# Optimization experiments

Measured on AMD Instinct MI355X. Metric: run time of the kernel, lower is better.

The kernel has to match this reference:

```python
import jax, jax.numpy as jnp
import numpy as np

N, IN, OUT, RANK = 8192, 4096, 4096, 16
SCALING = 2.0

def setup_inputs() -> dict:
    key = jax.random.key(0)
    k1, k2, k3, k4 = jax.random.split(key, 4)
    x = jax.random.normal(k1, (N, IN), dtype=jnp.float32)
    weight = jax.random.normal(k2, (OUT, IN), dtype=jnp.float32) * (1.0 / np.sqrt(IN))
    lora_A = jax.random.normal(k3, (RANK, IN), dtype=jnp.float32) * (1.0 / np.sqrt(IN))
    lora_B = jax.random.normal(k4, (OUT, RANK), dtype=jnp.float32) * 0.01
    return {"x": x, "weight": weight, "lora_A": lora_A, "lora_B": lora_B}

def reference(x, weight, lora_A, lora_B):
    # frozen base linear: F.linear(x, weight) == x @ weight.T  -> [N, OUT]
    base = jnp.einsum('ni,oi->no', x, weight)
    # LoRA branch: dropout(x) (p=0 => identity) @ A.T @ B.T, scaled
    lora = jnp.einsum('ni,ri->nr', x, lora_A)      # [N, RANK]
    lora = jnp.einsum('nr,or->no', lora, lora_B)   # [N, OUT]
    return base + lora * SCALING
```

## Files before the change

### kernel.cpp

```cpp
#include <hip/hip_runtime.h>


#define N_ROWS 8192
#define K_DIM  4096
#define N_COLS 4096
#define RANK   16
#define BK     64
#define NT     (K_DIM / BK)

typedef __bf16 bf16x8 __attribute__((ext_vector_type(8)));
typedef float  f32x4  __attribute__((ext_vector_type(4)));

__device__ __forceinline__ unsigned short f2bf(float f) {
  unsigned int u = __builtin_bit_cast(unsigned int, f);
  u += 0x7FFFu + ((u >> 16) & 1u);
  return (unsigned short)(u >> 16);
}


__global__ __launch_bounds__(256) void conv_x_kernel(const float* __restrict__ x,
                                                     unsigned short* __restrict__ xb) {
  size_t idx = (size_t)blockIdx.x * blockDim.x + threadIdx.x;
  const float4 v = *reinterpret_cast<const float4*>(x + idx * 4);
  ushort4 r;
  r.x = f2bf(v.x); r.y = f2bf(v.y); r.z = f2bf(v.z); r.w = f2bf(v.w);
  *reinterpret_cast<ushort4*>(xb + idx * 4) = r;
}

__global__ __launch_bounds__(256) void make_weff_kernel(const float* __restrict__ w,
                                                        const float* __restrict__ A,
                                                        const float* __restrict__ Bm,
                                                        unsigned short* __restrict__ wb) {
  size_t idx = (size_t)blockIdx.x * blockDim.x + threadIdx.x;
  int o  = (int)(idx >> 10);
  int ic = (int)(idx & 1023) << 2;
  const float4 wv = *reinterpret_cast<const float4*>(w + (size_t)o * K_DIM + ic);
  float a0 = wv.x, a1 = wv.y, a2 = wv.z, a3 = wv.w;
  float br[RANK];
#pragma unroll
  for (int r4 = 0; r4 < RANK / 4; ++r4) {
    const float4 bv = *reinterpret_cast<const float4*>(Bm + (size_t)o * RANK + r4 * 4);
    br[r4 * 4 + 0] = bv.x; br[r4 * 4 + 1] = bv.y;
    br[r4 * 4 + 2] = bv.z; br[r4 * 4 + 3] = bv.w;
  }
#pragma unroll
  for (int r = 0; r < RANK; ++r) {
    const float4 av = *reinterpret_cast<const float4*>(A + (size_t)r * K_DIM + ic);
    float b2 = br[r] * 2.0f;
    a0 += b2 * av.x; a1 += b2 * av.y; a2 += b2 * av.z; a3 += b2 * av.w;
  }
  ushort4 rr;
  rr.x = f2bf(a0); rr.y = f2bf(a1); rr.z = f2bf(a2); rr.w = f2bf(a3);
  *reinterpret_cast<ushort4*>(wb + (size_t)o * K_DIM + ic) = rr;
}


__device__ __forceinline__ void gload_lds16(const void* g, void* l) {
  __builtin_amdgcn_global_load_lds(
      (__attribute__((address_space(1))) void*)g,
      (__attribute__((address_space(3))) void*)l, 16, 0, 0);
}

__global__ __launch_bounds__(512, 1) void gemm_bf16_pipe(
    const unsigned short* __restrict__ xb, const unsigned short* __restrict__ wb,
    float* __restrict__ out) {
  __shared__ __align__(16) char smem[131072];

  const int t  = threadIdx.x;
  const int l  = t & 63;
  const int wv = t >> 6;
  const int lr = l & 15;
  const int lk = l >> 4;
  const int wr = wv >> 2;
  const int wc = wv & 3;

  const int bid  = blockIdx.x;
  const int sbid = (bid & 7) * 64 + (bid >> 3);
  const int bm   = sbid >> 4;
  const int bn   = sbid & 15;

  const int srow = t >> 3;
  const int scol = ((t & 7) ^ ((t >> 3) & 7)) << 3;
  const unsigned short* gA = xb + (size_t)(bm * 256 + srow) * K_DIM + scol;
  const unsigned short* gB = wb + (size_t)(bn * 256 + srow) * K_DIM + scol;
  char* ldsA = smem + t * 16;
  char* ldsB = smem + 65536 + t * 16;

#define STG_A(hh, SRC, NB) do {                                                 \
    const unsigned short* _g = (SRC) + (size_t)((hh) * 128) * K_DIM;            \
    char* _l = ldsA + (NB) + (hh) * 16384;                                      \
    gload_lds16(_g, _l);                                                        \
    gload_lds16(_g + (size_t)64 * K_DIM, _l + 8192);                            \
  } while (0)
#define STG_B(hh, SRC, NB) do {                                                 \
    const unsigned short* _g = (SRC) + (size_t)((hh) * 128) * K_DIM;            \
    char* _l = ldsB + (NB) + (hh) * 16384;                                      \
    gload_lds16(_g, _l);                                                        \
    gload_lds16(_g + (size_t)64 * K_DIM, _l + 8192);                            \
  } while (0)

  const int g0   = (lk ^ (lr & 7)) << 4;
  const int g1   = ((lk + 4) ^ (lr & 7)) << 4;
  const int aoff = (wr * 16 + lr) * 128;
  const int boff = (wc * 16 + lr) * 128;

  bf16x8 aE[8], aO[8], bO[4], bE[2][4];
  f32x4 acc[8][4];
#pragma unroll
  for (int m = 0; m < 8; ++m)
#pragma unroll
    for (int n = 0; n < 4; ++n)
      acc[m][n] = (f32x4){0.f, 0.f, 0.f, 0.f};

#define RD_A(DST, BASE) do {                                                    \
    _Pragma("unroll")                                                           \
    for (int m = 0; m < 4; ++m) {                                               \
      DST[2 * m + 0] = *(const bf16x8*)(smem + (BASE) + m * 4096 + aoff + g0);  \
      DST[2 * m + 1] = *(const bf16x8*)(smem + (BASE) + m * 4096 + aoff + g1);  \
    }                                                                           \
  } while (0)
#define RD_B(DST, BASE) do {                                                    \
    _Pragma("unroll")                                                           \
    for (int n = 0; n < 2; ++n) {                                               \
      DST[2 * n + 0] = *(const bf16x8*)(smem + 65536 + (BASE) + n * 8192 + boff + g0); \
      DST[2 * n + 1] = *(const bf16x8*)(smem + 65536 + (BASE) + n * 8192 + boff + g1); \
    }                                                                           \
  } while (0)

#define MFMA_Q(MB, AF, NB0, BF) do {                                            \
    _Pragma("unroll")                                                           \
    for (int mi = 0; mi < 4; ++mi)                                              \
      _Pragma("unroll")                                                         \
      for (int ni = 0; ni < 2; ++ni)                                            \
        _Pragma("unroll")                                                       \
        for (int kk = 0; kk < 2; ++kk)                                          \
          acc[(MB) + mi][(NB0) + ni] = __builtin_amdgcn_mfma_f32_16x16x32_bf16( \
              AF[mi * 2 + kk], BF[ni * 2 + kk], acc[(MB) + mi][(NB0) + ni], 0, 0, 0); \
  } while (0)

#define PH_BAR() do {                                                           \
    __builtin_amdgcn_sched_barrier(0);                                          \
    __builtin_amdgcn_s_barrier();                                               \
    __builtin_amdgcn_sched_barrier(0);                                          \
  } while (0)
#define PH_BAR_VM(VM) do {                                                      \
    __builtin_amdgcn_sched_barrier(0);                                          \
    asm volatile("s_waitcnt vmcnt(" #VM ")" ::: "memory");                      \
    __builtin_amdgcn_s_barrier();                                               \
    __builtin_amdgcn_sched_barrier(0);                                          \
  } while (0)

#define TILE(CB, NB, PC, PN, T) do {                                            \
    const int _tk = ((T) + 1 < NT) ? (T) + 1 : NT - 1;                          \
    const unsigned short* _sA = gA + (size_t)_tk * BK;                          \
    const unsigned short* _sB = gB + (size_t)_tk * BK;                          \
                                                                       \
    RD_B(bO, (CB) + 16384);                                                     \
    STG_A(0, _sA, NB); STG_A(1, _sA, NB);                                       \
    __builtin_amdgcn_s_setprio(1); MFMA_Q(0, aE, 0, bE[PC]);                    \
    __builtin_amdgcn_s_setprio(0);                                              \
    PH_BAR();                                                                   \
                                                                       \
    RD_A(aO, (CB) + 16384);                                                     \
    STG_B(0, _sB, NB); STG_B(1, _sB, NB);                                       \
    __builtin_amdgcn_s_setprio(1); MFMA_Q(0, aE, 2, bO);                        \
    __builtin_amdgcn_s_setprio(0);                                              \
    PH_BAR_VM(4);                                                               \
                                                                       \
    RD_A(aE, (NB));                                                             \
    __builtin_amdgcn_s_setprio(1); MFMA_Q(4, aO, 2, bO);                        \
    __builtin_amdgcn_s_setprio(0);                                              \
    PH_BAR_VM(2);                                                               \
                                                                       \
    RD_B(bE[PN], (NB));                                                         \
    __builtin_amdgcn_s_setprio(1); MFMA_Q(4, aO, 0, bE[PC]);                    \
    __builtin_amdgcn_s_setprio(0);                                              \
    PH_BAR_VM(0);                                                               \
  } while (0)

  STG_A(0, gA, 0); STG_A(1, gA, 0); STG_B(0, gB, 0); STG_B(1, gB, 0);
  __builtin_amdgcn_sched_barrier(0);
  asm volatile("s_waitcnt vmcnt(0)" ::: "memory");
  __builtin_amdgcn_s_barrier();
  __builtin_amdgcn_sched_barrier(0);
  RD_A(aE, 0);
  RD_B(bE[0], 0);

#pragma nounroll
  for (int u = 0; u < NT / 2; ++u) {
    TILE(0, 32768, 0, 1, 2 * u);
    TILE(32768, 0, 1, 0, 2 * u + 1);
  }

  const int orow = bm * 256 + wr * 16 + lk * 4;
  const int ocol = bn * 256 + wc * 16 + lr;
#pragma unroll
  for (int mf = 0; mf < 8; ++mf)
#pragma unroll
    for (int nf = 0; nf < 4; ++nf)
#pragma unroll
      for (int j = 0; j < 4; ++j)
        out[(size_t)(orow + mf * 32 + j) * N_COLS + (ocol + nf * 64)] = acc[mf][nf][j];

#undef STG_A
#undef STG_B
#undef RD_A
#undef RD_B
#undef MFMA_Q
#undef PH_BAR
#undef PH_BAR_VM
#undef TILE
}


__global__ __launch_bounds__(256) void fallback_kernel(const float* __restrict__ x,
                                                       const float* __restrict__ w,
                                                       const float* __restrict__ A,
                                                       const float* __restrict__ Bm,
                                                       float* __restrict__ out) {
  const int o    = blockIdx.x * 256 + threadIdx.x;
  const int nrow = blockIdx.y;
  float bro[RANK];
#pragma unroll
  for (int r = 0; r < RANK; ++r) bro[r] = Bm[(size_t)o * RANK + r] * 2.0f;
  float bacc = 0.f;
  float tacc[RANK];
#pragma unroll
  for (int r = 0; r < RANK; ++r) tacc[r] = 0.f;
  for (int k = 0; k < K_DIM; ++k) {
    float xv = x[(size_t)nrow * K_DIM + k];
    bacc += xv * w[(size_t)o * K_DIM + k];
#pragma unroll
    for (int r = 0; r < RANK; ++r) tacc[r] += xv * A[(size_t)r * K_DIM + k];
  }
  float res = bacc;
#pragma unroll
  for (int r = 0; r < RANK; ++r) res += bro[r] * tacc[r];
  out[(size_t)nrow * N_COLS + o] = res;
}


extern "C" void kernel_launch(void* const* d_in, const int* in_sizes, int n_in,
                              void* d_out, int out_size, void* d_ws, size_t ws_size,
                              hipStream_t stream) {
  const float* x  = (const float*)d_in[0];
  const float* w  = (const float*)d_in[1];
  const float* A  = (const float*)d_in[2];
  const float* Bm = (const float*)d_in[3];
  float* out = (float*)d_out;

  const size_t need = ((size_t)N_ROWS * K_DIM + (size_t)N_COLS * K_DIM) * sizeof(unsigned short);
  if (ws_size < need) {
    dim3 grid(N_COLS / 256, N_ROWS);
    fallback_kernel<<<grid, 256, 0, stream>>>(x, w, A, Bm, out);
    return;
  }

  unsigned short* xb = (unsigned short*)d_ws;
  unsigned short* wb = xb + (size_t)N_ROWS * K_DIM;

  conv_x_kernel<<<(N_ROWS * K_DIM / 4) / 256, 256, 0, stream>>>(x, xb);
  make_weff_kernel<<<(N_COLS * K_DIM / 4) / 256, 256, 0, stream>>>(w, A, Bm, wb);

  const int grid_gemm = (N_ROWS / 256) * (N_COLS / 256);
  gemm_bf16_pipe<<<grid_gemm, 512, 0, stream>>>(xb, wb, out);
}
```

Baseline: 333.3 us.

## Restructure GEMM main loop into two fat phases with full-register B fragments

Replaces the four-phase ping-pong register schedule, which overlapped LDS reads with MFMA through separate even/odd fragment buffers, with two larger phases per K-tile. Each phase loads A and all B fragments, waits on lgkmcnt(0), then runs 32 MFMAs over a half of the M fragments. Global-to-LDS staging for the next tile is reordered, with adjusted vmcnt waits. This cuts the number of barriers per tile but exposes LDS read latency before each MFMA burst, since reads are no longer prefetched into alternate registers.

```diff
diff --git a/kernel.cpp b/kernel.cpp
--- a/kernel.cpp
+++ b/kernel.cpp
@@ -61,7 +61,7 @@
       (__attribute__((address_space(3))) void*)l, 16, 0, 0);
 }
 
-__global__ __launch_bounds__(512, 1) void gemm_bf16_pipe(
+__global__ __launch_bounds__(512, 1) void gemm_bf16_fat(
     const unsigned short* __restrict__ xb, const unsigned short* __restrict__ wb,
     float* __restrict__ out) {
   __shared__ __align__(16) char smem[131072];
@@ -104,7 +104,8 @@
   const int aoff = (wr * 16 + lr) * 128;
   const int boff = (wc * 16 + lr) * 128;
 
-  bf16x8 aE[8], aO[8], bO[4], bE[2][4];
+  bf16x8 aF[8];
+  bf16x8 bF[8];
   f32x4 acc[8][4];
 #pragma unroll
   for (int m = 0; m < 8; ++m)
@@ -112,85 +113,82 @@
     for (int n = 0; n < 4; ++n)
       acc[m][n] = (f32x4){0.f, 0.f, 0.f, 0.f};
 
-#define RD_A(DST, BASE) do {                                                    \
+#define RD_A(BASE) do {                                                         \
     _Pragma("unroll")                                                           \
     for (int m = 0; m < 4; ++m) {                                               \
-      DST[2 * m + 0] = *(const bf16x8*)(smem + (BASE) + m * 4096 + aoff + g0);  \
-      DST[2 * m + 1] = *(const bf16x8*)(smem + (BASE) + m * 4096 + aoff + g1);  \
+      aF[2 * m + 0] = *(const bf16x8*)(smem + (BASE) + m * 4096 + aoff + g0);   \
+      aF[2 * m + 1] = *(const bf16x8*)(smem + (BASE) + m * 4096 + aoff + g1);   \
     }                                                                           \
   } while (0)
-#define RD_B(DST, BASE) do {                                                    \
+#define RD_B(hh, BASE) do {                                                     \
     _Pragma("unroll")                                                           \
     for (int n = 0; n < 2; ++n) {                                               \
-      DST[2 * n + 0] = *(const bf16x8*)(smem + 65536 + (BASE) + n * 8192 + boff + g0); \
-      DST[2 * n + 1] = *(const bf16x8*)(smem + 65536 + (BASE) + n * 8192 + boff + g1); \
+      bF[4 * (hh) + 2 * n + 0] =                                                \
+        *(const bf16x8*)(smem + 65536 + (BASE) + (hh) * 16384 + n * 8192 + boff + g0); \
+      bF[4 * (hh) + 2 * n + 1] =                                                \
+        *(const bf16x8*)(smem + 65536 + (BASE) + (hh) * 16384 + n * 8192 + boff + g1); \
     }                                                                           \
   } while (0)
 
-#define MFMA_Q(MB, AF, NB0, BF) do {                                            \
+#define MFMA_H(MB) do {                                                         \
     _Pragma("unroll")                                                           \
     for (int mi = 0; mi < 4; ++mi)                                              \
       _Pragma("unroll")                                                         \
-      for (int ni = 0; ni < 2; ++ni)                                            \
+      for (int ni = 0; ni < 4; ++ni)                                            \
         _Pragma("unroll")                                                       \
         for (int kk = 0; kk < 2; ++kk)                                          \
-          acc[(MB) + mi][(NB0) + ni] = __builtin_amdgcn_mfma_f32_16x16x32_bf16( \
-              AF[mi * 2 + kk], BF[ni * 2 + kk], acc[(MB) + mi][(NB0) + ni], 0, 0, 0); \
-  } while (0)
-
-#define PH_BAR() do {                                                           \
+          acc[(MB) + mi][ni] = __builtin_amdgcn_mfma_f32_16x16x32_bf16(         \
+              aF[mi * 2 + kk], bF[ni * 2 + kk], acc[(MB) + mi][ni], 0, 0, 0);   \
+  } while (0)
+
+#define PH_PRE() do {                                                           \
     __builtin_amdgcn_sched_barrier(0);                                          \
     __builtin_amdgcn_s_barrier();                                               \
-    __builtin_amdgcn_sched_barrier(0);                                          \
-  } while (0)
-#define PH_BAR_VM(VM) do {                                                      \
+    asm volatile("s_waitcnt lgkmcnt(0)" ::: "memory");                          \
+    __builtin_amdgcn_sched_barrier(0);                                          \
+    __builtin_amdgcn_s_setprio(1);                                              \
+  } while (0)
+#define PH_POST_VM(VM) do {                                                     \
+    __builtin_amdgcn_s_setprio(0);                                              \
     __builtin_amdgcn_sched_barrier(0);                                          \
     asm volatile("s_waitcnt vmcnt(" #VM ")" ::: "memory");                      \
     __builtin_amdgcn_s_barrier();                                               \
     __builtin_amdgcn_sched_barrier(0);                                          \
   } while (0)
 
-#define TILE(CB, NB, PC, PN, T) do {                                            \
+#define TILE(CB, NB, T) do {                                                    \
     const int _tk = ((T) + 1 < NT) ? (T) + 1 : NT - 1;                          \
     const unsigned short* _sA = gA + (size_t)_tk * BK;                          \
     const unsigned short* _sB = gB + (size_t)_tk * BK;                          \
                                                                        \
-    RD_B(bO, (CB) + 16384);                                                     \
-    STG_A(0, _sA, NB); STG_A(1, _sA, NB);                                       \
-    __builtin_amdgcn_s_setprio(1); MFMA_Q(0, aE, 0, bE[PC]);                    \
-    __builtin_amdgcn_s_setprio(0);                                              \
-    PH_BAR();                                                                   \
+    RD_A((CB));                                                                 \
+    RD_B(0, (CB)); RD_B(1, (CB));                                               \
+    STG_A(0, _sA, NB); STG_B(0, _sB, NB); STG_B(1, _sB, NB);                    \
+    PH_PRE();                                                                   \
+    MFMA_H(0);                                                                  \
+    PH_POST_VM(6);                                                              \
                                                                        \
-    RD_A(aO, (CB) + 16384);                                                     \
-    STG_B(0, _sB, NB); STG_B(1, _sB, NB);                                       \
-    __builtin_amdgcn_s_setprio(1); MFMA_Q(0, aE, 2, bO);                        \
-    __builtin_amdgcn_s_setprio(0);                                              \
-    PH_BAR_VM(4);                                                               \
-                                                                       \
-    RD_A(aE, (NB));                                                             \
-    __builtin_amdgcn_s_setprio(1); MFMA_Q(4, aO, 2, bO);                        \
-    __builtin_amdgcn_s_setprio(0);                                              \
-    PH_BAR_VM(2);                                                               \
-                                                                       \
-    RD_B(bE[PN], (NB));                                                         \
-    __builtin_amdgcn_s_setprio(1); MFMA_Q(4, aO, 0, bE[PC]);                    \
-    __builtin_amdgcn_s_setprio(0);                                              \
-    PH_BAR_VM(0);                                                               \
-  } while (0)
-
-  STG_A(0, gA, 0); STG_A(1, gA, 0); STG_B(0, gB, 0); STG_B(1, gB, 0);
+    RD_A((CB) + 16384);                                                         \
+    STG_A(1, _sA, NB);                                                          \
+    PH_PRE();                                                                   \
+    MFMA_H(4);                                                                  \
+    PH_POST_VM(2);                                                              \
+  } while (0)
+
+  STG_A(0, gA, 0); STG_B(0, gB, 0); STG_B(1, gB, 0);
+  STG_A(1, gA, 0);
   __builtin_amdgcn_sched_barrier(0);
-  asm volatile("s_waitcnt vmcnt(0)" ::: "memory");
+  asm volatile("s_waitcnt vmcnt(2)" ::: "memory");
   __builtin_amdgcn_s_barrier();
   __builtin_amdgcn_sched_barrier(0);
-  RD_A(aE, 0);
-  RD_B(bE[0], 0);
 
 #pragma nounroll
   for (int u = 0; u < NT / 2; ++u) {
-    TILE(0, 32768, 0, 1, 2 * u);
-    TILE(32768, 0, 1, 0, 2 * u + 1);
-  }
+    TILE(0, 32768, 2 * u);
+    TILE(32768, 0, 2 * u + 1);
+  }
+
+  asm volatile("s_waitcnt vmcnt(0)" ::: "memory");
 
   const int orow = bm * 256 + wr * 16 + lk * 4;
   const int ocol = bn * 256 + wc * 16 + lr;
@@ -206,9 +204,9 @@
 #undef STG_B
 #undef RD_A
 #undef RD_B
-#undef MFMA_Q
-#undef PH_BAR
-#undef PH_BAR_VM
+#undef MFMA_H
+#undef PH_PRE
+#undef PH_POST_VM
 #undef TILE
 }
 
@@ -263,5 +261,5 @@
   make_weff_kernel<<<(N_COLS * K_DIM / 4) / 256, 256, 0, stream>>>(w, A, Bm, wb);
 
   const int grid_gemm = (N_ROWS / 256) * (N_COLS / 256);
-  gemm_bf16_pipe<<<grid_gemm, 512, 0, stream>>>(xb, wb, out);
-}
+  gemm_bf16_fat<<<grid_gemm, 512, 0, stream>>>(xb, wb, out);
+}
```

Result: faster. 318.6 us (-4.4%).

## Reorder GEMM tile staging and relax vmcnt waits for deeper load lookahead

Applied to the files above, without the earlier changes.

Reorders the global-to-LDS staging within each K tile so that A(0) and both B halves are issued in the first phase and A(1) in the second. Every phase now ends with a partial vmcnt wait of 6, 6, 4 or 2 instead of 0, 4, 2 or 0, so prefetches stay in flight across phase and tile boundaries. It adds sched_barriers after the staging and read issue, and a final vmcnt(0) drain before the epilogue. The aim is to hide more global-memory latency behind MFMA work. The risk is that the looser waits and the removed memory clobbers could let LDS reads run before their data has landed.

```diff
diff --git a/kernel.cpp b/kernel.cpp
--- a/kernel.cpp
+++ b/kernel.cpp
@@ -61,7 +61,7 @@
       (__attribute__((address_space(3))) void*)l, 16, 0, 0);
 }
 
-__global__ __launch_bounds__(512, 1) void gemm_bf16_pipe(
+__global__ __launch_bounds__(512, 1) void gemm_bf16_look(
     const unsigned short* __restrict__ xb, const unsigned short* __restrict__ wb,
     float* __restrict__ out) {
   __shared__ __align__(16) char smem[131072];
@@ -138,14 +138,9 @@
               AF[mi * 2 + kk], BF[ni * 2 + kk], acc[(MB) + mi][(NB0) + ni], 0, 0, 0); \
   } while (0)
 
-#define PH_BAR() do {                                                           \
-    __builtin_amdgcn_sched_barrier(0);                                          \
-    __builtin_amdgcn_s_barrier();                                               \
-    __builtin_amdgcn_sched_barrier(0);                                          \
-  } while (0)
-#define PH_BAR_VM(VM) do {                                                      \
-    __builtin_amdgcn_sched_barrier(0);                                          \
-    asm volatile("s_waitcnt vmcnt(" #VM ")" ::: "memory");                      \
+#define PH_END(VM) do {                                                         \
+    __builtin_amdgcn_sched_barrier(0);                                          \
+    asm volatile("s_waitcnt vmcnt(" #VM ")");                                   \
     __builtin_amdgcn_s_barrier();                                               \
     __builtin_amdgcn_sched_barrier(0);                                          \
   } while (0)
@@ -154,33 +149,37 @@
     const int _tk = ((T) + 1 < NT) ? (T) + 1 : NT - 1;                          \
     const unsigned short* _sA = gA + (size_t)_tk * BK;                          \
     const unsigned short* _sB = gB + (size_t)_tk * BK;                          \
-                                                                       \
+                     \
     RD_B(bO, (CB) + 16384);                                                     \
-    STG_A(0, _sA, NB); STG_A(1, _sA, NB);                                       \
+    STG_A(0, _sA, NB); STG_B(0, _sB, NB); STG_B(1, _sB, NB);                    \
+    __builtin_amdgcn_sched_barrier(0);                                          \
     __builtin_amdgcn_s_setprio(1); MFMA_Q(0, aE, 0, bE[PC]);                    \
     __builtin_amdgcn_s_setprio(0);                                              \
-    PH_BAR();                                                                   \
-                                                                       \
+    PH_END(6);                                                                  \
+                               \
     RD_A(aO, (CB) + 16384);                                                     \
-    STG_B(0, _sB, NB); STG_B(1, _sB, NB);                                       \
+    STG_A(1, _sA, NB);                                                          \
+    __builtin_amdgcn_sched_barrier(0);                                          \
     __builtin_amdgcn_s_setprio(1); MFMA_Q(0, aE, 2, bO);                        \
     __builtin_amdgcn_s_setprio(0);                                              \
-    PH_BAR_VM(4);                                                               \
-                                                                       \
+    PH_END(6);                                                                  \
+                                            \
     RD_A(aE, (NB));                                                             \
+    __builtin_amdgcn_sched_barrier(0);                                          \
     __builtin_amdgcn_s_setprio(1); MFMA_Q(4, aO, 2, bO);                        \
     __builtin_amdgcn_s_setprio(0);                                              \
-    PH_BAR_VM(2);                                                               \
-                                                                       \
+    PH_END(4);                                                                  \
+                                    \
     RD_B(bE[PN], (NB));                                                         \
+    __builtin_amdgcn_sched_barrier(0);                                          \
     __builtin_amdgcn_s_setprio(1); MFMA_Q(4, aO, 0, bE[PC]);                    \
     __builtin_amdgcn_s_setprio(0);                                              \
-    PH_BAR_VM(0);                                                               \
+    PH_END(2);                                                                  \
   } while (0)
 
   STG_A(0, gA, 0); STG_A(1, gA, 0); STG_B(0, gB, 0); STG_B(1, gB, 0);
   __builtin_amdgcn_sched_barrier(0);
-  asm volatile("s_waitcnt vmcnt(0)" ::: "memory");
+  asm volatile("s_waitcnt vmcnt(0)");
   __builtin_amdgcn_s_barrier();
   __builtin_amdgcn_sched_barrier(0);
   RD_A(aE, 0);
@@ -191,6 +190,8 @@
     TILE(0, 32768, 0, 1, 2 * u);
     TILE(32768, 0, 1, 0, 2 * u + 1);
   }
+
+  asm volatile("s_waitcnt vmcnt(0)");
 
   const int orow = bm * 256 + wr * 16 + lk * 4;
   const int ocol = bn * 256 + wc * 16 + lr;
@@ -207,8 +208,7 @@
 #undef RD_A
 #undef RD_B
 #undef MFMA_Q
-#undef PH_BAR
-#undef PH_BAR_VM
+#undef PH_END
 #undef TILE
 }
 
@@ -263,5 +263,5 @@
   make_weff_kernel<<<(N_COLS * K_DIM / 4) / 256, 256, 0, stream>>>(w, A, Bm, wb);
 
   const int grid_gemm = (N_ROWS / 256) * (N_COLS / 256);
-  gemm_bf16_pipe<<<grid_gemm, 512, 0, stream>>>(xb, wb, out);
-}
+  gemm_bf16_look<<<grid_gemm, 512, 0, stream>>>(xb, wb, out);
+}
```

After: 349.9 us. 1.05x slower.
